# Optimization experiments

Hardware: AMD Instinct MI355X
Metric: run time of the kernel (lower is better)

## Reference

```python
import jax, jax.numpy as jnp
import numpy as np

U, M, E, EL, H, F, C = 200000, 100000, 2000000, 500000, 64, 20, 7


def setup_inputs() -> dict:
    key = jax.random.key(0)
    ks = jax.random.split(key, 20)
    s = 0.02
    return {
        "user_node_id": jnp.arange(U, dtype=jnp.int64),
        "movie_node_id": jnp.arange(M, dtype=jnp.int64),
        "movie_x": jax.random.normal(ks[0], (M, F), jnp.float32),
        "edge_src": jax.random.randint(ks[1], (E,), 0, U),
        "edge_dst": jax.random.randint(ks[2], (E,), 0, M),
        "el_src": jax.random.randint(ks[3], (EL,), 0, U),
        "el_dst": jax.random.randint(ks[4], (EL,), 0, M),
        "user_emb": jax.random.normal(ks[5], (U, H), jnp.float32) * s,
        "movie_emb": jax.random.normal(ks[6], (M, H), jnp.float32) * s,
        "w_movie": jax.random.normal(ks[7], (F, H), jnp.float32) * s,
        "b_movie": jnp.zeros((H,), jnp.float32),
        "l1_rates_Wl": jax.random.normal(ks[8], (H, H), jnp.float32) * s,
        "l1_rates_bl": jnp.zeros((H,), jnp.float32),
        "l1_rates_Wr": jax.random.normal(ks[9], (H, H), jnp.float32) * s,
        "l1_rev_Wl": jax.random.normal(ks[10], (H, H), jnp.float32) * s,
        "l1_rev_bl": jnp.zeros((H,), jnp.float32),
        "l1_rev_Wr": jax.random.normal(ks[11], (H, H), jnp.float32) * s,
        "l2_rates_Wl": jax.random.normal(ks[12], (H, H), jnp.float32) * s,
        "l2_rates_bl": jnp.zeros((H,), jnp.float32),
        "l2_rates_Wr": jax.random.normal(ks[13], (H, H), jnp.float32) * s,
        "l2_rev_Wl": jax.random.normal(ks[14], (H, H), jnp.float32) * s,
        "l2_rev_bl": jnp.zeros((H,), jnp.float32),
        "l2_rev_Wr": jax.random.normal(ks[15], (H, H), jnp.float32) * s,
        "cls_W": jax.random.normal(ks[16], (2 * H, C), jnp.float32) * s,
        "cls_b": jnp.zeros((C,), jnp.float32),
    }


def _sage(x_src, x_dst, src, dst, n_dst, Wl, bl, Wr):
    # mean-aggregate neighbor messages: gather -> segment_sum -> divide by degree
    msg = x_src[src]                                            # [E, H]
    agg = jax.ops.segment_sum(msg, dst, num_segments=n_dst)     # [n_dst, H]
    deg = jax.ops.segment_sum(jnp.ones((src.shape[0],), x_src.dtype), dst,
                              num_segments=n_dst)
    agg = agg / jnp.maximum(deg, 1.0)[:, None]
    return agg @ Wl + bl + x_dst @ Wr                           # SAGEConv: lin_l(aggr) + lin_r(root)


def reference(user_node_id, movie_node_id, movie_x, edge_src, edge_dst,
              el_src, el_dst, user_emb, movie_emb, w_movie, b_movie,
              l1_rates_Wl, l1_rates_bl, l1_rates_Wr,
              l1_rev_Wl, l1_rev_bl, l1_rev_Wr,
              l2_rates_Wl, l2_rates_bl, l2_rates_Wr,
              l2_rev_Wl, l2_rev_bl, l2_rev_Wr,
              cls_W, cls_b):
    # input projections
    x_user = user_emb[user_node_id]                              # [U, H]
    x_movie = movie_x @ w_movie + b_movie + movie_emb[movie_node_id]  # [M, H]

    # hetero GNN layer 1 (relu)
    u1 = jax.nn.relu(_sage(x_movie, x_user, edge_dst, edge_src, x_user.shape[0],
                           l1_rev_Wl, l1_rev_bl, l1_rev_Wr))
    m1 = jax.nn.relu(_sage(x_user, x_movie, edge_src, edge_dst, x_movie.shape[0],
                           l1_rates_Wl, l1_rates_bl, l1_rates_Wr))
    # hetero GNN layer 2 (no activation)
    u2 = _sage(m1, u1, edge_dst, edge_src, u1.shape[0],
               l2_rev_Wl, l2_rev_bl, l2_rev_Wr)
    m2 = _sage(u1, m1, edge_src, edge_dst, m1.shape[0],
               l2_rates_Wl, l2_rates_bl, l2_rates_Wr)

    # edge classifier over labeled (user, movie) pairs
    edge_feat = jnp.concatenate([u2[el_src], m2[el_dst]], axis=-1)  # [EL, 2H]
    return edge_feat @ cls_W + cls_b                                # [EL, C]
```

## Files before the change

### kernel.cpp

```cpp
#include <hip/hip_runtime.h>
#include <cstdint>
#include <cstddef>

#define H 64
#define C 7
#define F 20
#define BSH 9
#define BSZ 512
#define CH 8192

typedef unsigned short u16;
typedef __attribute__((ext_vector_type(8))) short bf16x8;
typedef __attribute__((ext_vector_type(4))) float f32x4;

static __device__ __forceinline__ int imax(int a, int b) { return a > b ? a : b; }
static __device__ __forceinline__ int imin(int a, int b) { return a < b ? a : b; }

static __device__ __forceinline__ float bf2f(u16 v) {
  union { unsigned u; float f; } x; x.u = ((unsigned)v) << 16; return x.f;
}
static __device__ __forceinline__ u16 f2bf(float f) {
  union { float f; unsigned u; } x; x.f = f;
  unsigned r = x.u + 0x7fffu + ((x.u >> 16) & 1u);
  return (u16)(r >> 16);
}
static __device__ __forceinline__ int pack2bf(float a, float b) {
  return (int)f2bf(a) | ((int)f2bf(b) << 16);
}
static __device__ __forceinline__ float lo16f(unsigned v) {
  union { unsigned u; float f; } x; x.u = v << 16; return x.f;
}
static __device__ __forceinline__ float hi16f(unsigned v) {
  union { unsigned u; float f; } x; x.u = v & 0xffff0000u; return x.f;
}

__global__ __launch_bounds__(256) void k_bhist(const int* __restrict__ esrc,
                                               const int* __restrict__ edst, int E,
                                               int* __restrict__ gcnt_u, int* __restrict__ gcnt_m,
                                               int nbu, int nbm) {
  extern __shared__ int sh[];
  int* hu = sh;
  int* hm = sh + nbu;
  for (int i = threadIdx.x; i < nbu + nbm; i += 256) sh[i] = 0;
  __syncthreads();
  int stride = gridDim.x * 256;
  for (int i = blockIdx.x * 256 + threadIdx.x; i < E; i += stride) {
    atomicAdd(&hu[esrc[i] >> BSH], 1);
    atomicAdd(&hm[edst[i] >> BSH], 1);
  }
  __syncthreads();
  for (int i = threadIdx.x; i < nbu; i += 256) if (hu[i]) atomicAdd(&gcnt_u[i], hu[i]);
  for (int i = threadIdx.x; i < nbm; i += 256) if (hm[i]) atomicAdd(&gcnt_m[i], hm[i]);
}

__global__ __launch_bounds__(256) void k_bscan(const int* __restrict__ gcnt_u,
                                               const int* __restrict__ gcnt_m,
                                               int nbu, int nbm, int E,
                                               int* __restrict__ boff_u, int* __restrict__ boff_m,
                                               int* __restrict__ gcur_u, int* __restrict__ gcur_m) {
  __shared__ int s[1024];
  for (int i = threadIdx.x; i < nbu; i += 256) s[i] = gcnt_u[i];
  for (int i = threadIdx.x; i < nbm; i += 256) s[512 + i] = gcnt_m[i];
  __syncthreads();
  if (threadIdx.x == 0) {
    int r = 0;
    for (int i = 0; i < nbu; ++i) { int v = s[i]; s[i] = r; r += v; }
  }
  if (threadIdx.x == 1) {
    int r = 0;
    for (int i = 0; i < nbm; ++i) { int v = s[512 + i]; s[512 + i] = r; r += v; }
  }
  __syncthreads();
  for (int i = threadIdx.x; i < nbu; i += 256) { boff_u[i] = s[i]; gcur_u[i] = s[i]; }
  for (int i = threadIdx.x; i < nbm; i += 256) { boff_m[i] = s[512 + i]; gcur_m[i] = s[512 + i]; }
  if (threadIdx.x == 0) { boff_u[nbu] = E; boff_m[nbm] = E; }
}

__global__ __launch_bounds__(256) void k_bscat(const int* __restrict__ esrc,
                                               const int* __restrict__ edst, int E,
                                               int* __restrict__ gcur_u, int* __restrict__ gcur_m,
                                               unsigned int* __restrict__ pk_u,
                                               unsigned int* __restrict__ pk_m,
                                               int nbu, int nbm, int nchunks) {
  extern __shared__ int sh2[];
  int dir = (blockIdx.x >= (unsigned)nchunks) ? 1 : 0;
  int chunk = dir ? (blockIdx.x - nchunks) : blockIdx.x;
  const int* key = dir ? edst : esrc;
  const int* pay = dir ? esrc : edst;
  int* gcur = dir ? gcur_m : gcur_u;
  unsigned int* pk = dir ? pk_m : pk_u;
  int nb = dir ? nbm : nbu;
  int* cnt = sh2;
  int* base = sh2 + nb;
  int beg = chunk * CH;
  int end = imin(beg + CH, E);
  for (int i = threadIdx.x; i < nb; i += 256) cnt[i] = 0;
  __syncthreads();
  for (int i = beg + threadIdx.x; i < end; i += 256) atomicAdd(&cnt[key[i] >> BSH], 1);
  __syncthreads();
  for (int i = threadIdx.x; i < nb; i += 256) {
    int c = cnt[i];
    base[i] = c ? atomicAdd(&gcur[i], c) : 0;
    cnt[i] = 0;
  }
  __syncthreads();
  for (int i = beg + threadIdx.x; i < end; i += 256) {
    int k = key[i];
    int b = k >> BSH;
    int r = atomicAdd(&cnt[b], 1);
    pk[base[b] + r] = ((unsigned)(k & (BSZ - 1)) << 18) | (unsigned)pay[i];
  }
}

__global__ __launch_bounds__(512) void k_bbuild(const unsigned int* __restrict__ pk_u,
                                                const unsigned int* __restrict__ pk_m,
                                                const int* __restrict__ boff_u,
                                                const int* __restrict__ boff_m,
                                                int nbu, int nbm, int U_, int M_, int E,
                                                int* __restrict__ csr_u, int* __restrict__ csr_m,
                                                int* __restrict__ off_u, int* __restrict__ off_m) {
  __shared__ int hist[BSZ];
  __shared__ int cur[BSZ];
  int dir = (blockIdx.x >= (unsigned)nbu) ? 1 : 0;
  int b = dir ? (blockIdx.x - nbu) : blockIdx.x;
  const unsigned int* pk = dir ? pk_m : pk_u;
  const int* boff = dir ? boff_m : boff_u;
  int N = dir ? M_ : U_;
  int nb = dir ? nbm : nbu;
  int* csr = dir ? csr_m : csr_u;
  int* off = dir ? off_m : off_u;
  int beg = boff[b], end = boff[b + 1];
  int t = threadIdx.x;
  hist[t] = 0;
  __syncthreads();
  for (int i = beg + t; i < end; i += 512) atomicAdd(&hist[pk[i] >> 18], 1);
  __syncthreads();
  int v0 = hist[t];
  for (int o = 1; o < 512; o <<= 1) {
    int x = (t >= o) ? hist[t - o] : 0;
    __syncthreads();
    hist[t] += x;
    __syncthreads();
  }
  int excl = hist[t] - v0;
  cur[t] = excl;
  int node = (b << BSH) + t;
  if (node < N) off[node] = beg + excl;
  if (t == 0 && b == nb - 1) off[N] = E;
  __syncthreads();
  for (int i = beg + t; i < end; i += 512) {
    unsigned int p = pk[i];
    int n = (int)(p >> 18);
    int r = atomicAdd(&cur[n], 1);
    csr[beg + r] = (int)(p & 0x3FFFFu);
  }
}

__global__ __launch_bounds__(256) void k_prep(
    const float* __restrict__ movie_x, const float* __restrict__ w_movie,
    const float* __restrict__ b_movie, const float* __restrict__ movie_emb,
    const int* __restrict__ mnid,
    const float* __restrict__ user_emb, const int* __restrict__ unid,
    const float* __restrict__ l2u_Wl, const float* __restrict__ l2u_Wr,
    const float* __restrict__ l2u_bl,
    const float* __restrict__ l2m_Wl, const float* __restrict__ l2m_Wr,
    const float* __restrict__ l2m_bl,
    const float* __restrict__ clsW,
    u16* __restrict__ xm_bf, u16* __restrict__ xu_bf, float* __restrict__ cw,
    int M_, int U_, int gProj, int gCvt) {
  __shared__ float ws_[F * H];
  int b = blockIdx.x;
  if (b < gProj) {
    for (int i = threadIdx.x; i < F * H; i += 256) ws_[i] = w_movie[i];
    __syncthreads();
    int t = b * 256 + threadIdx.x;
    int m = t >> 6;
    int h = t & 63;
    if (m >= M_) return;
    float acc = b_movie[h] + movie_emb[(size_t)mnid[m] * H + h];
    const float* xr = movie_x + (size_t)m * F;
    #pragma unroll
    for (int f = 0; f < F; ++f) acc += xr[f] * ws_[f * H + h];
    xm_bf[(size_t)m * H + h] = f2bf(acc);
  } else if (b < gProj + gCvt) {
    int t = (b - gProj) * 256 + threadIdx.x;
    if (t >= U_ * 16) return;
    int i = t >> 4;
    int g = t & 15;
    const float4 v = *(const float4*)(user_emb + (size_t)unid[i] * H + g * 4);
    ushort4 o;
    o.x = f2bf(v.x); o.y = f2bf(v.y); o.z = f2bf(v.z); o.w = f2bf(v.w);
    *(ushort4*)(xu_bf + (size_t)i * H + g * 4) = o;
  } else {
    int t = (b - gProj - gCvt) * 256 + threadIdx.x;
    if (t < 448) {
      int k = t / C, c = t % C;
      float s = 0.f;
      for (int j = 0; j < H; ++j) s += l2u_Wl[k * H + j] * clsW[j * C + c];
      cw[t] = s;
    } else if (t < 896) {
      int u = t - 448; int k = u / C, c = u % C;
      float s = 0.f;
      for (int j = 0; j < H; ++j) s += l2u_Wr[k * H + j] * clsW[j * C + c];
      cw[t] = s;
    } else if (t < 1344) {
      int u = t - 896; int k = u / C, c = u % C;
      float s = 0.f;
      for (int j = 0; j < H; ++j) s += l2m_Wl[k * H + j] * clsW[(H + j) * C + c];
      cw[t] = s;
    } else if (t < 1792) {
      int u = t - 1344; int k = u / C, c = u % C;
      float s = 0.f;
      for (int j = 0; j < H; ++j) s += l2m_Wr[k * H + j] * clsW[(H + j) * C + c];
      cw[t] = s;
    } else if (t < 1799) {
      int c = t - 1792;
      float s = 0.f;
      for (int j = 0; j < H; ++j) s += l2u_bl[j] * clsW[j * C + c];
      cw[t] = s;
    } else if (t < 1806) {
      int c = t - 1799;
      float s = 0.f;
      for (int j = 0; j < H; ++j) s += l2m_bl[j] * clsW[(H + j) * C + c];
      cw[t] = s;
    }
  }
}

__global__ __launch_bounds__(512, 4) void k_sage_mfma(
    const u16* __restrict__ xu, const u16* __restrict__ xm,
    const int* __restrict__ csr_u, const int* __restrict__ off_u,
    const int* __restrict__ csr_m, const int* __restrict__ off_m,
    const float* __restrict__ WlU, const float* __restrict__ blU, const float* __restrict__ WrU,
    const float* __restrict__ WlM, const float* __restrict__ blM, const float* __restrict__ WrM,
    const float* __restrict__ CWml, const float* __restrict__ CWur,
    const float* __restrict__ CWul, const float* __restrict__ CWmr,
    u16* __restrict__ Zu, u16* __restrict__ Zm,
    int U_, int M_, int E_, int gU) {
  __shared__ int sWl[64 * 36];
  __shared__ int sWr[64 * 36];
  __shared__ int sAggHi[128 * 36];
  __shared__ int sAggLo[128 * 36];
  __shared__ float sCl[448];
  __shared__ float sCr[448];
  __shared__ float sBl[64];

  int movie = (blockIdx.x >= (unsigned)gU) ? 1 : 0;
  int bside = movie ? (blockIdx.x - gU) : blockIdx.x;
  const u16* srcT = movie ? xu : xm;
  const u16* rootT = movie ? xm : xu;
  const int* csr = movie ? csr_m : csr_u;
  const int* off = movie ? off_m : off_u;
  const float* Wl = movie ? WlM : WlU;
  const float* Wr = movie ? WrM : WrU;
  const float* bl = movie ? blM : blU;
  const float* CWl = movie ? CWul : CWml;
  const float* CWr = movie ? CWmr : CWur;
  u16* Z = movie ? Zm : Zu;
  int N = movie ? M_ : U_;

  int tid = threadIdx.x;
  for (int idx = tid; idx < 2048; idx += 512) {
    int j = idx & 63, kk = idx >> 6;
    sWl[j * 36 + kk] = pack2bf(Wl[(2 * kk) * H + j], Wl[(2 * kk + 1) * H + j]);
    sWr[j * 36 + kk] = pack2bf(Wr[(2 * kk) * H + j], Wr[(2 * kk + 1) * H + j]);
  }
  for (int idx = tid; idx < 448; idx += 512) { sCl[idx] = CWl[idx]; sCr[idx] = CWr[idx]; }
  if (tid < 64) sBl[tid] = bl[tid];
  __syncthreads();

  int lane = tid & 63;
  int wid = tid >> 6;
  int slot = lane >> 3;
  int l3 = lane & 7;
  int sbase = slot * 8;
  int node0 = bside * 128 + wid * 16;

  #pragma unroll
  for (int g = 0; g < 2; ++g) {
    int n = node0 + g * 8 + slot;
    int nc = n < N ? n : N - 1;
    int jb = off[nc];
    int d = off[nc + 1] - jb;
    if (n >= N) d = 0;
    int dm1 = imax(d - 1, 0);
    int dmax = d;
    dmax = imax(dmax, __shfl_xor(dmax, 8));
    dmax = imax(dmax, __shfl_xor(dmax, 16));
    dmax = imax(dmax, __shfl_xor(dmax, 32));

    float acc[8] = {0.f, 0.f, 0.f, 0.f, 0.f, 0.f, 0.f, 0.f};
    for (int tb = 0; tb < dmax; tb += 8) {
      int ci = jb + imin(tb + l3, dm1);
      ci = imin(ci, E_ - 1);
      int e = csr[ci];
      uint4 v[8];
      #pragma unroll
      for (int k = 0; k < 8; ++k) {
        int a = __shfl(e, sbase + k);
        v[k] = *(const uint4*)(srcT + (size_t)(unsigned)a * H + l3 * 8);
      }
      #pragma unroll
      for (int k = 0; k < 8; ++k) {
        float mk = (tb + k < d) ? 1.0f : 0.0f;
        acc[0] = fmaf(lo16f(v[k].x), mk, acc[0]);
        acc[1] = fmaf(hi16f(v[k].x), mk, acc[1]);
        acc[2] = fmaf(lo16f(v[k].y), mk, acc[2]);
        acc[3] = fmaf(hi16f(v[k].y), mk, acc[3]);
        acc[4] = fmaf(lo16f(v[k].z), mk, acc[4]);
        acc[5] = fmaf(hi16f(v[k].z), mk, acc[5]);
        acc[6] = fmaf(lo16f(v[k].w), mk, acc[6]);
        acc[7] = fmaf(hi16f(v[k].w), mk, acc[7]);
      }
    }

    float inv = 1.0f / (float)imax(d, 1);
    int hi4[4], lo4[4];
    #pragma unroll
    for (int pp = 0; pp < 4; ++pp) {
      float s0 = acc[2 * pp] * inv;
      float s1 = acc[2 * pp + 1] * inv;
      u16 b0 = f2bf(s0), b1 = f2bf(s1);
      float r0 = s0 - bf2f(b0), r1 = s1 - bf2f(b1);
      hi4[pp] = (int)b0 | ((int)b1 << 16);
      lo4[pp] = pack2bf(r0, r1);
    }
    int row = wid * 16 + g * 8 + slot;
    *(int4*)&sAggHi[row * 36 + l3 * 4] = *(int4*)hi4;
    *(int4*)&sAggLo[row * 36 + l3 * 4] = *(int4*)lo4;
  }

  int r16 = lane & 15;
  int q4 = lane >> 4;
  union FU { int4 i; bf16x8 b; };
  FU ahi[2], alo[2], art[2];
  int arow = wid * 16 + r16;
  int rnode = node0 + r16;
  rnode = rnode < N ? rnode : N - 1;
  #pragma unroll
  for (int kt = 0; kt < 2; ++kt) {
    ahi[kt].i = *(const int4*)&sAggHi[arow * 36 + kt * 16 + q4 * 4];
    alo[kt].i = *(const int4*)&sAggLo[arow * 36 + kt * 16 + q4 * 4];
    art[kt].i = ((const int4*)(rootT + (size_t)rnode * H))[kt * 4 + q4];
  }
  float val[4][4];
  #pragma unroll
  for (int t = 0; t < 4; ++t) {
    f32x4 cacc = {0.f, 0.f, 0.f, 0.f};
    #pragma unroll
    for (int kt = 0; kt < 2; ++kt) {
      FU bwl, bwr;
      bwl.i = *(const int4*)&sWl[(t * 16 + r16) * 36 + kt * 16 + q4 * 4];
      bwr.i = *(const int4*)&sWr[(t * 16 + r16) * 36 + kt * 16 + q4 * 4];
      cacc = __builtin_amdgcn_mfma_f32_16x16x32_bf16(ahi[kt].b, bwl.b, cacc, 0, 0, 0);
      cacc = __builtin_amdgcn_mfma_f32_16x16x32_bf16(alo[kt].b, bwl.b, cacc, 0, 0, 0);
      cacc = __builtin_amdgcn_mfma_f32_16x16x32_bf16(art[kt].b, bwr.b, cacc, 0, 0, 0);
    }
    float bj = sBl[t * 16 + r16];
    #pragma unroll
    for (int r = 0; r < 4; ++r) val[t][r] = fmaxf(cacc[r] + bj, 0.f);
  }

  float zacc[4] = {0.f, 0.f, 0.f, 0.f};
  #pragma unroll
  for (int c = 0; c < C; ++c) {
    float tl[4], tr[4];
    #pragma unroll
    for (int r = 0; r < 4; ++r) {
      tl[r] = val[0][r] * sCl[(r16) * C + c] + val[1][r] * sCl[(16 + r16) * C + c] +
              val[2][r] * sCl[(32 + r16) * C + c] + val[3][r] * sCl[(48 + r16) * C + c];
      tr[r] = val[0][r] * sCr[(r16) * C + c] + val[1][r] * sCr[(16 + r16) * C + c] +
              val[2][r] * sCr[(32 + r16) * C + c] + val[3][r] * sCr[(48 + r16) * C + c];
    }
    #pragma unroll
    for (int o = 1; o < 16; o <<= 1) {
      #pragma unroll
      for (int r = 0; r < 4; ++r) {
        tl[r] += __shfl_xor(tl[r], o);
        tr[r] += __shfl_xor(tr[r], o);
      }
    }
    #pragma unroll
    for (int r = 0; r < 4; ++r) {
      zacc[r] = (r16 == c) ? zacc[r] + tl[r] : zacc[r];
      zacc[r] = (r16 == 8 + c) ? zacc[r] + tr[r] : zacc[r];
    }
  }
  #pragma unroll
  for (int r = 0; r < 4; ++r) {
    int node = node0 + q4 * 4 + r;
    if (node < N) Z[(size_t)node * 16 + r16] = f2bf(zacc[r]);
  }
}

__global__ __launch_bounds__(256) void k_agg7m(
    const u16* __restrict__ Zu, const u16* __restrict__ Zm,
    const int* __restrict__ csr_u, const int* __restrict__ off_u,
    const int* __restrict__ csr_m, const int* __restrict__ off_m,
    const float* __restrict__ cbu, const float* __restrict__ cbm,
    float* __restrict__ Pu, float* __restrict__ Pm,
    int U_, int M_, int gU) {
  int movie = (blockIdx.x >= (unsigned)gU) ? 1 : 0;
  int bside = movie ? (blockIdx.x - gU) : blockIdx.x;
  const u16* Zsrc = movie ? Zu : Zm;
  const u16* Zroot = movie ? Zm : Zu;
  const int* csr = movie ? csr_m : csr_u;
  const int* off = movie ? off_m : off_u;
  const float* cb = movie ? cbm : cbu;
  float* P = movie ? Pm : Pu;
  int N = movie ? M_ : U_;

  int n = bside * 256 + threadIdx.x;
  if (n >= N) return;
  int beg = off[n], end = off[n + 1];
  float acc[8] = {0.f, 0.f, 0.f, 0.f, 0.f, 0.f, 0.f, 0.f};
  for (int j = beg; j < end; ++j) {
    int a = csr[j];
    uint4 z = *(const uint4*)(Zsrc + (size_t)a * 16);
    acc[0] += lo16f(z.x); acc[1] += hi16f(z.x);
    acc[2] += lo16f(z.y); acc[3] += hi16f(z.y);
    acc[4] += lo16f(z.z); acc[5] += hi16f(z.z);
    acc[6] += lo16f(z.w); acc[7] += hi16f(z.w);
  }
  float inv = 1.f / (float)imax(end - beg, 1);
  uint4 zr = *(const uint4*)(Zroot + (size_t)n * 16 + 8);
  float4 o0, o1;
  o0.x = acc[0] * inv + lo16f(zr.x) + cb[0];
  o0.y = acc[1] * inv + hi16f(zr.x) + cb[1];
  o0.z = acc[2] * inv + lo16f(zr.y) + cb[2];
  o0.w = acc[3] * inv + hi16f(zr.y) + cb[3];
  o1.x = acc[4] * inv + lo16f(zr.z) + cb[4];
  o1.y = acc[5] * inv + hi16f(zr.z) + cb[5];
  o1.z = acc[6] * inv + lo16f(zr.w) + cb[6];
  o1.w = 0.f;
  float4* po = (float4*)(P + (size_t)n * 8);
  po[0] = o0;
  po[1] = o1;
}

__global__ void k_final(const int* __restrict__ els, const int* __restrict__ eld,
                        const float* __restrict__ Pu, const float* __restrict__ Pm,
                        const float* __restrict__ clsb, float* __restrict__ out, int total) {
  int t = blockIdx.x * 256 + threadIdx.x;
  if (t >= total) return;
  int e = t / C, c = t - e * C;
  out[t] = Pu[(size_t)els[e] * 8 + c] + Pm[(size_t)eld[e] * 8 + c] + clsb[c];
}

extern "C" void kernel_launch(void* const* d_in, const int* in_sizes, int n_in,
                              void* d_out, int out_size, void* d_ws, size_t ws_size,
                              hipStream_t stream) {
  (void)n_in; (void)out_size; (void)ws_size;
  const int*   unid      = (const int*)d_in[0];
  const int*   mnid      = (const int*)d_in[1];
  const float* movie_x   = (const float*)d_in[2];
  const int*   e_src     = (const int*)d_in[3];
  const int*   e_dst     = (const int*)d_in[4];
  const int*   el_src    = (const int*)d_in[5];
  const int*   el_dst    = (const int*)d_in[6];
  const float* user_emb  = (const float*)d_in[7];
  const float* movie_emb = (const float*)d_in[8];
  const float* w_movie   = (const float*)d_in[9];
  const float* b_movie   = (const float*)d_in[10];
  const float* l1r_Wl    = (const float*)d_in[11];
  const float* l1r_bl    = (const float*)d_in[12];
  const float* l1r_Wr    = (const float*)d_in[13];
  const float* l1v_Wl    = (const float*)d_in[14];
  const float* l1v_bl    = (const float*)d_in[15];
  const float* l1v_Wr    = (const float*)d_in[16];
  const float* l2r_Wl    = (const float*)d_in[17];
  const float* l2r_bl    = (const float*)d_in[18];
  const float* l2r_Wr    = (const float*)d_in[19];
  const float* l2v_Wl    = (const float*)d_in[20];
  const float* l2v_bl    = (const float*)d_in[21];
  const float* l2v_Wr    = (const float*)d_in[22];
  const float* cls_W     = (const float*)d_in[23];
  const float* cls_b     = (const float*)d_in[24];

  int U  = in_sizes[0];
  int M  = in_sizes[1];
  int E  = in_sizes[3];
  int EL = in_sizes[5];

  int nbu = (U + BSZ - 1) / BSZ;
  int nbm = (M + BSZ - 1) / BSZ;
  int nchunks = (E + CH - 1) / CH;

  char* p = (char*)d_ws;
  auto alloc = [&](size_t nbytes) { char* r = p; p += (nbytes + 255) & ~(size_t)255; return r; };

  u16*   xm_bf  = (u16*)alloc((size_t)M * H * 2);
  u16*   xu_bf  = (u16*)alloc((size_t)U * H * 2);
  u16*   Zu     = (u16*)alloc((size_t)U * 16 * 2);
  u16*   Zm     = (u16*)alloc((size_t)M * 16 * 2);
  float* Pu     = (float*)alloc((size_t)U * 8 * 4);
  float* Pm     = (float*)alloc((size_t)M * 8 * 4);
  int*   csr_u  = (int*)alloc((size_t)E * 4);
  int*   csr_m  = (int*)alloc((size_t)E * 4);
  int*   off_u  = (int*)alloc((size_t)(U + 1) * 4);
  int*   off_m  = (int*)alloc((size_t)(M + 1) * 4);
  unsigned int* pk_u = (unsigned int*)alloc((size_t)E * 4);
  unsigned int* pk_m = (unsigned int*)alloc((size_t)E * 4);
  int*   gcnt   = (int*)alloc((size_t)(nbu + nbm) * 4);
  int*   gcnt_u = gcnt;
  int*   gcnt_m = gcnt + nbu;
  int*   boff_u = (int*)alloc((size_t)(nbu + 1) * 4);
  int*   boff_m = (int*)alloc((size_t)(nbm + 1) * 4);
  int*   gcur_u = (int*)alloc((size_t)nbu * 4);
  int*   gcur_m = (int*)alloc((size_t)nbm * 4);
  float* cw     = (float*)alloc(1806 * 4);
  float* CWul = cw, *CWur = cw + 448, *CWml = cw + 896, *CWmr = cw + 1344;
  float* cbu  = cw + 1792, *cbm = cw + 1799;

  hipMemsetAsync(gcnt, 0, (size_t)(nbu + nbm) * 4, stream);

  k_bhist<<<256, 256, (size_t)(nbu + nbm) * 4, stream>>>(e_src, e_dst, E, gcnt_u, gcnt_m, nbu, nbm);
  k_bscan<<<1, 256, 0, stream>>>(gcnt_u, gcnt_m, nbu, nbm, E, boff_u, boff_m, gcur_u, gcur_m);
  k_bscat<<<2 * nchunks, 256, (size_t)(2 * nbu) * 4, stream>>>(e_src, e_dst, E, gcur_u, gcur_m,
                                                               pk_u, pk_m, nbu, nbm, nchunks);
  k_bbuild<<<nbu + nbm, 512, 0, stream>>>(pk_u, pk_m, boff_u, boff_m, nbu, nbm, U, M, E,
                                          csr_u, csr_m, off_u, off_m);

  int gProj = (M * H + 255) / 256;
  int gCvt  = (U * 16 + 255) / 256;
  k_prep<<<gProj + gCvt + 8, 256, 0, stream>>>(
      movie_x, w_movie, b_movie, movie_emb, mnid, user_emb, unid,
      l2v_Wl, l2v_Wr, l2v_bl, l2r_Wl, l2r_Wr, l2r_bl, cls_W,
      xm_bf, xu_bf, cw, M, U, gProj, gCvt);

  int gU_s = (U + 127) / 128;
  int gM_s = (M + 127) / 128;
  k_sage_mfma<<<gU_s + gM_s, 512, 0, stream>>>(
      xu_bf, xm_bf, csr_u, off_u, csr_m, off_m,
      l1v_Wl, l1v_bl, l1v_Wr,
      l1r_Wl, l1r_bl, l1r_Wr,
      CWml, CWur, CWul, CWmr,
      Zu, Zm, U, M, E, gU_s);

  int gU_a = (U + 255) / 256;
  int gM_a = (M + 255) / 256;
  k_agg7m<<<gU_a + gM_a, 256, 0, stream>>>(Zu, Zm, csr_u, off_u, csr_m, off_m,
                                           cbu, cbm, Pu, Pm, U, M, gU_a);

  int total = EL * C;
  k_final<<<(total + 255) / 256, 256, 0, stream>>>(el_src, el_dst, Pu, Pm, cls_b, (float*)d_out, total);
}
```

Before: 525.6 us.

## Use MFMA for classifier projection and zero-row padding for masked gathers

```diff
diff --git a/kernel.cpp b/kernel.cpp
--- a/kernel.cpp
+++ b/kernel.cpp
@@ -12,6 +12,7 @@
 typedef unsigned short u16;
 typedef __attribute__((ext_vector_type(8))) short bf16x8;
 typedef __attribute__((ext_vector_type(4))) float f32x4;
+typedef __attribute__((ext_vector_type(2))) float f32x2;
 
 static __device__ __forceinline__ int imax(int a, int b) { return a > b ? a : b; }
 static __device__ __forceinline__ int imin(int a, int b) { return a < b ? a : b; }
@@ -32,6 +33,11 @@
 }
 static __device__ __forceinline__ float hi16f(unsigned v) {
   union { unsigned u; float f; } x; x.u = v & 0xffff0000u; return x.f;
+}
+static __device__ __forceinline__ int cvtpk_bf16(float a, float b) {
+  int w;
+  asm("v_cvt_pk_bf16_f32 %0, %1, %2" : "=v"(w) : "v"(a), "v"(b));
+  return w;
 }
 
 __global__ __launch_bounds__(256) void k_bhist(const int* __restrict__ esrc,
@@ -223,6 +229,10 @@
       float s = 0.f;
       for (int j = 0; j < H; ++j) s += l2m_bl[j] * clsW[(H + j) * C + c];
       cw[t] = s;
+    } else if (t < 1870) {
+      xm_bf[(size_t)M_ * H + (t - 1806)] = 0;
+    } else if (t < 1934) {
+      xu_bf[(size_t)U_ * H + (t - 1870)] = 0;
     }
   }
 }
@@ -241,8 +251,7 @@
   __shared__ int sWr[64 * 36];
   __shared__ int sAggHi[128 * 36];
   __shared__ int sAggLo[128 * 36];
-  __shared__ float sCl[448];
-  __shared__ float sCr[448];
+  __shared__ int sCC[16 * 36];
   __shared__ float sBl[64];
 
   int movie = (blockIdx.x >= (unsigned)gU) ? 1 : 0;
@@ -258,6 +267,7 @@
   const float* CWr = movie ? CWmr : CWur;
   u16* Z = movie ? Zm : Zu;
   int N = movie ? M_ : U_;
+  int zrow = movie ? U_ : M_;
 
   int tid = threadIdx.x;
   for (int idx = tid; idx < 2048; idx += 512) {
@@ -265,7 +275,15 @@
     sWl[j * 36 + kk] = pack2bf(Wl[(2 * kk) * H + j], Wl[(2 * kk + 1) * H + j]);
     sWr[j * 36 + kk] = pack2bf(Wr[(2 * kk) * H + j], Wr[(2 * kk + 1) * H + j]);
   }
-  for (int idx = tid; idx < 448; idx += 512) { sCl[idx] = CWl[idx]; sCr[idx] = CWr[idx]; }
+  for (int idx = tid; idx < 512; idx += 512) {
+    int cc = idx >> 5, kk = idx & 31;
+    float f0, f1;
+    if (cc < 7)       { f0 = CWl[(2 * kk) * C + cc];     f1 = CWl[(2 * kk + 1) * C + cc]; }
+    else if (cc == 7) { f0 = 0.f; f1 = 0.f; }
+    else if (cc < 15) { f0 = CWr[(2 * kk) * C + cc - 8]; f1 = CWr[(2 * kk + 1) * C + cc - 8]; }
+    else              { f0 = 0.f; f1 = 0.f; }
+    sCC[cc * 36 + kk] = pack2bf(f0, f1);
+  }
   if (tid < 64) sBl[tid] = bl[tid];
   __syncthreads();
 
@@ -283,17 +301,16 @@
     int jb = off[nc];
     int d = off[nc + 1] - jb;
     if (n >= N) d = 0;
-    int dm1 = imax(d - 1, 0);
     int dmax = d;
     dmax = imax(dmax, __shfl_xor(dmax, 8));
     dmax = imax(dmax, __shfl_xor(dmax, 16));
     dmax = imax(dmax, __shfl_xor(dmax, 32));
 
-    float acc[8] = {0.f, 0.f, 0.f, 0.f, 0.f, 0.f, 0.f, 0.f};
+    f32x2 acc2[4] = {{0.f, 0.f}, {0.f, 0.f}, {0.f, 0.f}, {0.f, 0.f}};
     for (int tb = 0; tb < dmax; tb += 8) {
-      int ci = jb + imin(tb + l3, dm1);
-      ci = imin(ci, E_ - 1);
-      int e = csr[ci];
+      int idx = tb + l3;
+      int ci = imin(jb + idx, E_ - 1);
+      int e = (idx < d) ? csr[ci] : zrow;
       uint4 v[8];
       #pragma unroll
       for (int k = 0; k < 8; ++k) {
@@ -302,15 +319,11 @@
       }
       #pragma unroll
       for (int k = 0; k < 8; ++k) {
-        float mk = (tb + k < d) ? 1.0f : 0.0f;
-        acc[0] = fmaf(lo16f(v[k].x), mk, acc[0]);
-        acc[1] = fmaf(hi16f(v[k].x), mk, acc[1]);
-        acc[2] = fmaf(lo16f(v[k].y), mk, acc[2]);
-        acc[3] = fmaf(hi16f(v[k].y), mk, acc[3]);
-        acc[4] = fmaf(lo16f(v[k].z), mk, acc[4]);
-        acc[5] = fmaf(hi16f(v[k].z), mk, acc[5]);
-        acc[6] = fmaf(lo16f(v[k].w), mk, acc[6]);
-        acc[7] = fmaf(hi16f(v[k].w), mk, acc[7]);
+        f32x2 p0 = {lo16f(v[k].x), hi16f(v[k].x)};
+        f32x2 p1 = {lo16f(v[k].y), hi16f(v[k].y)};
+        f32x2 p2 = {lo16f(v[k].z), hi16f(v[k].z)};
+        f32x2 p3 = {lo16f(v[k].w), hi16f(v[k].w)};
+        acc2[0] += p0; acc2[1] += p1; acc2[2] += p2; acc2[3] += p3;
       }
     }
 
@@ -318,12 +331,13 @@
     int hi4[4], lo4[4];
     #pragma unroll
     for (int pp = 0; pp < 4; ++pp) {
-      float s0 = acc[2 * pp] * inv;
-      float s1 = acc[2 * pp + 1] * inv;
-      u16 b0 = f2bf(s0), b1 = f2bf(s1);
-      float r0 = s0 - bf2f(b0), r1 = s1 - bf2f(b1);
-      hi4[pp] = (int)b0 | ((int)b1 << 16);
-      lo4[pp] = pack2bf(r0, r1);
+      float s0 = acc2[pp].x * inv;
+      float s1 = acc2[pp].y * inv;
+      int w = cvtpk_bf16(s0, s1);
+      float r0 = s0 - lo16f((unsigned)w);
+      float r1 = s1 - hi16f((unsigned)w);
+      hi4[pp] = w;
+      lo4[pp] = cvtpk_bf16(r0, r1);
     }
     int row = wid * 16 + g * 8 + slot;
     *(int4*)&sAggHi[row * 36 + l3 * 4] = *(int4*)hi4;
@@ -343,7 +357,10 @@
     alo[kt].i = *(const int4*)&sAggLo[arow * 36 + kt * 16 + q4 * 4];
     art[kt].i = ((const int4*)(rootT + (size_t)rnode * H))[kt * 4 + q4];
   }
-  float val[4][4];
+
+  u16* sVT = (u16*)(sAggHi + (size_t)wid * 16 * 36);
+  const int* sVTd = sAggHi + (size_t)wid * 16 * 36;
+
   #pragma unroll
   for (int t = 0; t < 4; ++t) {
     f32x4 cacc = {0.f, 0.f, 0.f, 0.f};
@@ -357,39 +374,31 @@
       cacc = __builtin_amdgcn_mfma_f32_16x16x32_bf16(art[kt].b, bwr.b, cacc, 0, 0, 0);
     }
     float bj = sBl[t * 16 + r16];
-    #pragma unroll
-    for (int r = 0; r < 4; ++r) val[t][r] = fmaxf(cacc[r] + bj, 0.f);
-  }
-
-  float zacc[4] = {0.f, 0.f, 0.f, 0.f};
+    float v0 = fmaxf(cacc[0] + bj, 0.f);
+    float v1 = fmaxf(cacc[1] + bj, 0.f);
+    float v2 = fmaxf(cacc[2] + bj, 0.f);
+    float v3 = fmaxf(cacc[3] + bj, 0.f);
+    int w01 = cvtpk_bf16(v0, v1);
+    int w23 = cvtpk_bf16(v2, v3);
+    int base = (q4 * 4) * 72 + t * 16 + r16;
+    sVT[base]       = (u16)w01;
+    sVT[base + 72]  = (u16)((unsigned)w01 >> 16);
+    sVT[base + 144] = (u16)w23;
+    sVT[base + 216] = (u16)((unsigned)w23 >> 16);
+  }
+
+  f32x4 z4 = {0.f, 0.f, 0.f, 0.f};
   #pragma unroll
-  for (int c = 0; c < C; ++c) {
-    float tl[4], tr[4];
-    #pragma unroll
-    for (int r = 0; r < 4; ++r) {
-      tl[r] = val[0][r] * sCl[(r16) * C + c] + val[1][r] * sCl[(16 + r16) * C + c] +
-              val[2][r] * sCl[(32 + r16) * C + c] + val[3][r] * sCl[(48 + r16) * C + c];
-      tr[r] = val[0][r] * sCr[(r16) * C + c] + val[1][r] * sCr[(16 + r16) * C + c] +
-              val[2][r] * sCr[(32 + r16) * C + c] + val[3][r] * sCr[(48 + r16) * C + c];
-    }
-    #pragma unroll
-    for (int o = 1; o < 16; o <<= 1) {
-      #pragma unroll
-      for (int r = 0; r < 4; ++r) {
-        tl[r] += __shfl_xor(tl[r], o);
-        tr[r] += __shfl_xor(tr[r], o);
-      }
-    }
-    #pragma unroll
-    for (int r = 0; r < 4; ++r) {
-      zacc[r] = (r16 == c) ? zacc[r] + tl[r] : zacc[r];
-      zacc[r] = (r16 == 8 + c) ? zacc[r] + tr[r] : zacc[r];
-    }
+  for (int kt = 0; kt < 2; ++kt) {
+    FU a2, b2;
+    a2.i = *(const int4*)&sVTd[r16 * 36 + kt * 16 + q4 * 4];
+    b2.i = *(const int4*)&sCC[r16 * 36 + kt * 16 + q4 * 4];
+    z4 = __builtin_amdgcn_mfma_f32_16x16x32_bf16(a2.b, b2.b, z4, 0, 0, 0);
   }
   #pragma unroll
   for (int r = 0; r < 4; ++r) {
     int node = node0 + q4 * 4 + r;
-    if (node < N) Z[(size_t)node * 16 + r16] = f2bf(zacc[r]);
+    if (node < N) Z[(size_t)node * 16 + r16] = f2bf(z4[r]);
   }
 }
 
@@ -489,8 +498,8 @@
   char* p = (char*)d_ws;
   auto alloc = [&](size_t nbytes) { char* r = p; p += (nbytes + 255) & ~(size_t)255; return r; };
 
-  u16*   xm_bf  = (u16*)alloc((size_t)M * H * 2);
-  u16*   xu_bf  = (u16*)alloc((size_t)U * H * 2);
+  u16*   xm_bf  = (u16*)alloc((size_t)(M + 1) * H * 2);
+  u16*   xu_bf  = (u16*)alloc((size_t)(U + 1) * H * 2);
   u16*   Zu     = (u16*)alloc((size_t)U * 16 * 2);
   u16*   Zm     = (u16*)alloc((size_t)M * 16 * 2);
   float* Pu     = (float*)alloc((size_t)U * 8 * 4);
```

After: 500.9 us. 1.05x faster.
